# Kernel tuning notes

Hardware: AMD Instinct MI355X
Metric: run time of the kernel (lower is better)

## Reference

```python
import jax, jax.numpy as jnp
import numpy as np

D = 768
H = 12
FF = 3072
B = 64
S = 197
NUM_ITERS = 5
DT = 0.1


def setup_inputs() -> dict:
    key = jax.random.key(0)
    ks = jax.random.split(key, 16)
    sc = 0.02
    inp = {
        'x': jax.random.normal(ks[0], (B, S, D), jnp.float32),
        # MultiheadAttention params (torch layout: in_proj_weight (3D, D))
        'in_proj_w': jax.random.normal(ks[1], (3 * D, D), jnp.float32) * sc,
        'in_proj_b': jnp.zeros((3 * D,), jnp.float32),
        'out_proj_w': jax.random.normal(ks[2], (D, D), jnp.float32) * sc,
        'out_proj_b': jnp.zeros((D,), jnp.float32),
        # LayerNorms
        'ln_attn_g': jnp.ones((D,), jnp.float32),
        'ln_attn_b': jnp.zeros((D,), jnp.float32),
        'ln1_g': jnp.ones((D,), jnp.float32),
        'ln1_b': jnp.zeros((D,), jnp.float32),
        'ln2_g': jnp.ones((D,), jnp.float32),
        'ln2_b': jnp.zeros((D,), jnp.float32),
        # INL dynamics MLP: Linear(D,D) -> GELU -> Linear(D,D)
        'inl_w1': jax.random.normal(ks[3], (D, D), jnp.float32) * sc,
        'inl_b1': jnp.zeros((D,), jnp.float32),
        'inl_w2': jax.random.normal(ks[4], (D, D), jnp.float32) * sc,
        'inl_b2': jnp.zeros((D,), jnp.float32),
        # FFN: Linear(D,FF) -> GELU -> Linear(FF,D)
        'ffn_w1': jax.random.normal(ks[5], (FF, D), jnp.float32) * sc,
        'ffn_b1': jnp.zeros((FF,), jnp.float32),
        'ffn_w2': jax.random.normal(ks[6], (D, FF), jnp.float32) * sc,
        'ffn_b2': jnp.zeros((D,), jnp.float32),
    }
    return inp


def _layernorm(x, g, b, eps=1e-5):
    mu = jnp.mean(x, axis=-1, keepdims=True)
    var = jnp.var(x, axis=-1, keepdims=True)
    return (x - mu) * jax.lax.rsqrt(var + eps) * g + b


def _mha(x, in_w, in_b, out_w, out_b):
    # x: (B,S,D); qkv projection per torch MultiheadAttention
    qkv = jnp.einsum('bsd,ed->bse', x, in_w) + in_b  # (B,S,3D)
    q, k, v = jnp.split(qkv, 3, axis=-1)
    dh = D // H
    q = q.reshape(q.shape[0], q.shape[1], H, dh)
    k = k.reshape(k.shape[0], k.shape[1], H, dh)
    v = v.reshape(v.shape[0], v.shape[1], H, dh)
    scores = jnp.einsum('bqhd,bkhd->bhqk', q, k) / jnp.sqrt(jnp.float32(dh))
    attn = jax.nn.softmax(scores, axis=-1)
    out = jnp.einsum('bhqk,bkhd->bqhd', attn, v)
    out = out.reshape(out.shape[0], out.shape[1], D)
    return jnp.einsum('bsd,ed->bse', out, out_w) + out_b


def _forward(x, in_proj_w, in_proj_b, out_proj_w, out_proj_b,
             ln_attn_g, ln_attn_b, ln1_g, ln1_b, ln2_g, ln2_b,
             inl_w1, inl_b1, inl_w2, inl_b2,
             ffn_w1, ffn_b1, ffn_w2, ffn_b2):
    xn = _layernorm(x, ln_attn_g, ln_attn_b)
    x = x + _mha(xn, in_proj_w, in_proj_b, out_proj_w, out_proj_b)

    # INL dynamics: 5-iter fixed-point loop on normalized state
    state = _layernorm(x, ln1_g, ln1_b)

    def step(state, _):
        h = jax.nn.gelu(jnp.einsum('bsd,ed->bse', state, inl_w1) + inl_b1,
                        approximate=False)
        delta = jnp.einsum('bse,de->bsd', h, inl_w2) + inl_b2
        return state + DT * delta, None

    state, _ = jax.lax.scan(step, state, None, length=NUM_ITERS)
    x = x + state

    # FFN
    xn2 = _layernorm(x, ln2_g, ln2_b)
    h = jax.nn.gelu(jnp.einsum('bsd,fd->bsf', xn2, ffn_w1) + ffn_b1,
                    approximate=False)
    x = x + jnp.einsum('bsf,df->bsd', h, ffn_w2) + ffn_b2
    return x


def reference(x, in_proj_w, in_proj_b, out_proj_w, out_proj_b,
              ln_attn_g, ln_attn_b, ln1_g, ln1_b, ln2_g, ln2_b,
              inl_w1, inl_b1, inl_w2, inl_b2,
              ffn_w1, ffn_b1, ffn_w2, ffn_b2):
    return _forward(x, in_proj_w, in_proj_b, out_proj_w, out_proj_b,
                    ln_attn_g, ln_attn_b, ln1_g, ln1_b, ln2_g, ln2_b,
                    inl_w1, inl_b1, inl_w2, inl_b2,
                    ffn_w1, ffn_b1, ffn_w2, ffn_b2)
```

## Files before the change

### kernel.cpp

```cpp
#include <hip/hip_runtime.h>
#include <hip/hip_bf16.h>
#include <cstdio>

typedef __bf16 bf16x4 __attribute__((ext_vector_type(4)));
typedef __bf16 bf16x8 __attribute__((ext_vector_type(8)));
typedef float  f32x4  __attribute__((ext_vector_type(4)));

#define NTOK 12608
#define DMODEL 768
#define SEQ 197

__device__ __forceinline__ float b2f(__bf16 v) { return (float)v; }

__device__ __forceinline__ float gelu_f(float x) {
    float y = 1.5957691216f * (x + 0.044715f * x * x * x);
    float e = __expf(y);
    float t = 1.f - 2.f / (e + 1.f);
    return 0.5f * x * (1.f + t);
}

__device__ __forceinline__ void gload16(const void* src, void* dst) {
    __builtin_amdgcn_global_load_lds(
        (const __attribute__((address_space(1))) void*)src,
        (__attribute__((address_space(3))) void*)dst,
        16, 0, 0);
}

struct CvtArgs {
    const float* src[6];
    __bf16* dst[6];
    int n4[6];
};
__global__ __launch_bounds__(256) void cvt_all_k(CvtArgs a)
{
#pragma unroll
    for (int t = 0; t < 6; ++t) {
        const float4* in = (const float4*)a.src[t];
        bf16x4* out = (bf16x4*)a.dst[t];
        const int n4 = a.n4[t];
        for (int i = blockIdx.x * 256 + threadIdx.x; i < n4; i += gridDim.x * 256) {
            float4 v = in[i];
            bf16x4 o;
            o[0] = (__bf16)v.x; o[1] = (__bf16)v.y; o[2] = (__bf16)v.z; o[3] = (__bf16)v.w;
            out[i] = o;
        }
    }
}

__global__ __launch_bounds__(256) void ln_k(const float* __restrict__ x,
                                            const float* __restrict__ g,
                                            const float* __restrict__ b,
                                            __bf16* __restrict__ out, int N)
{
    int wid = blockIdx.x * 4 + (threadIdx.x >> 6);
    if (wid >= N) return;
    int lane = threadIdx.x & 63;
    const float4* row = (const float4*)(x + (size_t)wid * DMODEL);
    float v[12];
    float s = 0.f, sq = 0.f;
#pragma unroll
    for (int j = 0; j < 3; ++j) {
        float4 u = row[lane + 64 * j];
        float f0 = u.x, f1 = u.y, f2 = u.z, f3 = u.w;
        v[j*4+0] = f0; v[j*4+1] = f1; v[j*4+2] = f2; v[j*4+3] = f3;
        s += f0 + f1 + f2 + f3;
        sq += f0*f0 + f1*f1 + f2*f2 + f3*f3;
    }
#pragma unroll
    for (int o = 32; o >= 1; o >>= 1) { s += __shfl_xor(s, o); sq += __shfl_xor(sq, o); }
    float mu = s * (1.f / DMODEL);
    float var = sq * (1.f / DMODEL) - mu * mu;
    float rstd = rsqrtf(var + 1e-5f);
    bf16x4* orow = (bf16x4*)(out + (size_t)wid * DMODEL);
    const float4* gg = (const float4*)g;
    const float4* bb = (const float4*)b;
#pragma unroll
    for (int j = 0; j < 3; ++j) {
        float4 gu = gg[lane + 64*j], bu = bb[lane + 64*j];
        bf16x4 o4;
        o4[0] = (__bf16)((v[j*4+0] - mu) * rstd * gu.x + bu.x);
        o4[1] = (__bf16)((v[j*4+1] - mu) * rstd * gu.y + bu.y);
        o4[2] = (__bf16)((v[j*4+2] - mu) * rstd * gu.z + bu.z);
        o4[3] = (__bf16)((v[j*4+3] - mu) * rstd * gu.w + bu.w);
        orow[lane + 64*j] = o4;
    }
}

__global__ __launch_bounds__(256) void addln_k(float* __restrict__ x1,
                                               const __bf16* __restrict__ st,
                                               const float* __restrict__ g,
                                               const float* __restrict__ b,
                                               __bf16* __restrict__ xn2, int N)
{
    int wid = blockIdx.x * 4 + (threadIdx.x >> 6);
    if (wid >= N) return;
    int lane = threadIdx.x & 63;
    float4* r1 = (float4*)(x1 + (size_t)wid * DMODEL);
    const bf16x4* r2 = (const bf16x4*)(st + (size_t)wid * DMODEL);
    float v[12];
    float s = 0.f, sq = 0.f;
#pragma unroll
    for (int j = 0; j < 3; ++j) {
        float4 u1 = r1[lane + 64*j];
        bf16x4 u2 = r2[lane + 64*j];
        float f0 = u1.x + b2f(u2[0]), f1 = u1.y + b2f(u2[1]);
        float f2 = u1.z + b2f(u2[2]), f3 = u1.w + b2f(u2[3]);
        v[j*4+0] = f0; v[j*4+1] = f1; v[j*4+2] = f2; v[j*4+3] = f3;
        s += f0 + f1 + f2 + f3;
        sq += f0*f0 + f1*f1 + f2*f2 + f3*f3;
        float4 o; o.x = f0; o.y = f1; o.z = f2; o.w = f3;
        r1[lane + 64*j] = o;
    }
#pragma unroll
    for (int o = 32; o >= 1; o >>= 1) { s += __shfl_xor(s, o); sq += __shfl_xor(sq, o); }
    float mu = s * (1.f / DMODEL);
    float var = sq * (1.f / DMODEL) - mu * mu;
    float rstd = rsqrtf(var + 1e-5f);
    bf16x4* on = (bf16x4*)(xn2 + (size_t)wid * DMODEL);
    const float4* gg = (const float4*)g;
    const float4* bb = (const float4*)b;
#pragma unroll
    for (int j = 0; j < 3; ++j) {
        float4 gu = gg[lane + 64*j], bu = bb[lane + 64*j];
        bf16x4 o4;
        o4[0] = (__bf16)((v[j*4+0] - mu) * rstd * gu.x + bu.x);
        o4[1] = (__bf16)((v[j*4+1] - mu) * rstd * gu.y + bu.y);
        o4[2] = (__bf16)((v[j*4+2] - mu) * rstd * gu.z + bu.z);
        o4[3] = (__bf16)((v[j*4+3] - mu) * rstd * gu.w + bu.w);
        on[lane + 64*j] = o4;
    }
}

template <int EPI>
__global__ __launch_bounds__(512) void gemm_k(const __bf16* __restrict__ A,
                                              const __bf16* __restrict__ W,
                                              const float* __restrict__ bias,
                                              const void* __restrict__ resv,
                                              void* __restrict__ outv,
                                              int Nv, int K)
{
    __shared__ __align__(16) __bf16 Al[2][64 * 64];
    __shared__ __align__(16) __bf16 Bl[2][128 * 64];
    const int tid = threadIdx.x;
    const int lane = tid & 63;
    const int wv = tid >> 6;
    const int wr = wv >> 2, wc = wv & 3;

    const int ncol = gridDim.x;
    const int nwg = ncol * gridDim.y;
    const int orig = blockIdx.x + ncol * blockIdx.y;
    const int q8 = nwg >> 3, r8 = nwg & 7;
    const int xcd = orig & 7, off8 = orig >> 3;
    const int wgid = (xcd < r8 ? xcd * (q8 + 1) : r8 * (q8 + 1) + (xcd - r8) * q8) + off8;
    const int bcol = (wgid % ncol) * 128;
    const int brow = (wgid / ncol) * 64;

    const int M = ncol * 128;
    const int srow = tid >> 3;
    const int scol = (tid & 7) * 8;
    const int sg = (((tid & 7) ^ (srow & 7)) << 3);
    const int lq = lane >> 4, lr = lane & 15;
    const int gsw = lr & 7;

    int ar = brow + srow; ar = ar < Nv ? ar : (Nv - 1);
    const __bf16* Arow = A + (size_t)ar * K + sg;
    const __bf16* Wrow[2];
#pragma unroll
    for (int it = 0; it < 2; ++it)
        Wrow[it] = W + (size_t)(bcol + it * 64 + srow) * K + sg;

    f32x4 acc[2][2];
#pragma unroll
    for (int m = 0; m < 2; ++m)
#pragma unroll
        for (int n = 0; n < 2; ++n)
#pragma unroll
            for (int i = 0; i < 4; ++i) acc[m][n][i] = 0.f;

    const int nk = K >> 6;

    gload16(Arow, &Al[0][srow * 64 + scol]);
#pragma unroll
    for (int it = 0; it < 2; ++it)
        gload16(Wrow[it], &Bl[0][(it * 64 + srow) * 64 + scol]);
    __syncthreads();

    for (int t = 0; t < nk; ++t) {
        const int cur = t & 1;
        if (t + 1 < nk) {
            const int koff = (t + 1) << 6;
            gload16(Arow + koff, &Al[cur ^ 1][srow * 64 + scol]);
#pragma unroll
            for (int it = 0; it < 2; ++it)
                gload16(Wrow[it] + koff, &Bl[cur ^ 1][(it * 64 + srow) * 64 + scol]);
        }
#pragma unroll
        for (int kk = 0; kk < 2; ++kk) {
            bf16x8 af[2], bfr[2];
            const int cg = ((kk * 4 + lq) ^ gsw) << 3;
#pragma unroll
            for (int m = 0; m < 2; ++m)
                af[m] = *(const bf16x8*)&Al[cur][(wr * 32 + m * 16 + lr) * 64 + cg];
#pragma unroll
            for (int n = 0; n < 2; ++n)
                bfr[n] = *(const bf16x8*)&Bl[cur][(wc * 32 + n * 16 + lr) * 64 + cg];
#pragma unroll
            for (int m = 0; m < 2; ++m)
#pragma unroll
                for (int n = 0; n < 2; ++n)
                    acc[m][n] = __builtin_amdgcn_mfma_f32_16x16x32_bf16(af[m], bfr[n], acc[m][n], 0, 0, 0);
        }
        __syncthreads();
    }

#pragma unroll
    for (int m = 0; m < 2; ++m) {
        int row0 = brow + wr * 32 + m * 16 + lq * 4;
#pragma unroll
        for (int n = 0; n < 2; ++n) {
            int col = bcol + wc * 32 + n * 16 + lr;
            float bv = bias[col];
#pragma unroll
            for (int i = 0; i < 4; ++i) {
                int row = row0 + i;
                if (row < Nv) {
                    float v = acc[m][n][i] + bv;
                    size_t off = (size_t)row * M + col;
                    if constexpr (EPI == 0) {
                        ((__bf16*)outv)[off] = (__bf16)v;
                    } else if constexpr (EPI == 1) {
                        ((float*)outv)[off] = v + ((const float*)resv)[off];
                    } else if constexpr (EPI == 2) {
                        ((__bf16*)outv)[off] = (__bf16)gelu_f(v);
                    } else {
                        ((__bf16*)outv)[off] = (__bf16)(b2f(((const __bf16*)resv)[off]) + 0.1f * v);
                    }
                }
            }
        }
    }
}

template <int EPI>
__global__ __launch_bounds__(512) void gemm_s(const __bf16* __restrict__ A,
                                              const __bf16* __restrict__ W,
                                              const float* __restrict__ bias,
                                              const void* __restrict__ resv,
                                              void* __restrict__ outv,
                                              int Nv, int K)
{
    __shared__ __align__(16) __bf16 Al[2][64 * 64];
    __shared__ __align__(16) __bf16 Bl[2][64 * 64];
    const int tid = threadIdx.x;
    const int lane = tid & 63;
    const int wv = tid >> 6;
    const int wr = wv >> 1, wc = wv & 1;

    const int ncol = gridDim.x;
    const int nwg = ncol * gridDim.y;
    const int orig = blockIdx.x + ncol * blockIdx.y;
    const int q8 = nwg >> 3, r8 = nwg & 7;
    const int xcd = orig & 7, off8 = orig >> 3;
    const int wgid = (xcd < r8 ? xcd * (q8 + 1) : r8 * (q8 + 1) + (xcd - r8) * q8) + off8;
    const int bcol = (wgid % ncol) * 64;
    const int brow = (wgid / ncol) * 64;

    const int M = ncol * 64;
    const int srow = tid >> 3;
    const int scol = (tid & 7) * 8;
    const int sg = (((tid & 7) ^ (srow & 7)) << 3);
    const int lq = lane >> 4, lr = lane & 15;
    const int gsw = lr & 7;

    int ar = brow + srow; ar = ar < Nv ? ar : (Nv - 1);
    const __bf16* Arow = A + (size_t)ar * K + sg;
    const __bf16* Wrow = W + (size_t)(bcol + srow) * K + sg;

    f32x4 acc[2];
#pragma unroll
    for (int n = 0; n < 2; ++n)
#pragma unroll
        for (int i = 0; i < 4; ++i) acc[n][i] = 0.f;

    const int nk = K >> 6;

    gload16(Arow, &Al[0][srow * 64 + scol]);
    gload16(Wrow, &Bl[0][srow * 64 + scol]);
    __syncthreads();

    for (int t = 0; t < nk; ++t) {
        const int cur = t & 1;
        if (t + 1 < nk) {
            const int koff = (t + 1) << 6;
            gload16(Arow + koff, &Al[cur ^ 1][srow * 64 + scol]);
            gload16(Wrow + koff, &Bl[cur ^ 1][srow * 64 + scol]);
        }
#pragma unroll
        for (int kk = 0; kk < 2; ++kk) {
            const int cg = ((kk * 4 + lq) ^ gsw) << 3;
            bf16x8 af = *(const bf16x8*)&Al[cur][(wr * 16 + lr) * 64 + cg];
            bf16x8 bfr[2];
#pragma unroll
            for (int n = 0; n < 2; ++n)
                bfr[n] = *(const bf16x8*)&Bl[cur][(wc * 32 + n * 16 + lr) * 64 + cg];
#pragma unroll
            for (int n = 0; n < 2; ++n)
                acc[n] = __builtin_amdgcn_mfma_f32_16x16x32_bf16(af, bfr[n], acc[n], 0, 0, 0);
        }
        __syncthreads();
    }

    {
        int row0 = brow + wr * 16 + lq * 4;
#pragma unroll
        for (int n = 0; n < 2; ++n) {
            int col = bcol + wc * 32 + n * 16 + lr;
            float bv = bias[col];
#pragma unroll
            for (int i = 0; i < 4; ++i) {
                int row = row0 + i;
                if (row < Nv) {
                    float v = acc[n][i] + bv;
                    size_t off = (size_t)row * M + col;
                    if constexpr (EPI == 0) {
                        ((__bf16*)outv)[off] = (__bf16)v;
                    } else if constexpr (EPI == 1) {
                        ((float*)outv)[off] = v + ((const float*)resv)[off];
                    } else if constexpr (EPI == 2) {
                        ((__bf16*)outv)[off] = (__bf16)gelu_f(v);
                    } else {
                        ((__bf16*)outv)[off] = (__bf16)(b2f(((const __bf16*)resv)[off]) + 0.1f * v);
                    }
                }
            }
        }
    }
}

__global__ __launch_bounds__(256) void attn_k(const __bf16* __restrict__ qkv,
                                              __bf16* __restrict__ attn_out)
{
    constexpr int S = SEQ, LDP = 232, QKVW = 2304;
    __shared__ __align__(16) __bf16 Vt[64 * LDP];
    __shared__ __align__(16) __bf16 P[4][16 * LDP];
    const int bh = blockIdx.x >> 1;
    const int half = blockIdx.x & 1;
    const int b = bh / 12, h = bh % 12;
    const size_t base = (size_t)b * S * QKVW;
    const int tid = threadIdx.x, lane = tid & 63, wv = tid >> 6;
    const int lq = lane >> 4, lr = lane & 15;

    for (int idx = tid; idx < 224 * 8; idx += 256) {
        int j = idx >> 3, d0 = (idx & 7) * 8;
        bf16x8 v8;
        if (j < S) v8 = *(const bf16x8*)(qkv + base + (size_t)j * QKVW + 1536 + h * 64 + d0);
        else {
#pragma unroll
            for (int e = 0; e < 8; ++e) v8[e] = (__bf16)0.f;
        }
#pragma unroll
        for (int e = 0; e < 8; ++e) Vt[(d0 + e) * LDP + j] = v8[e];
    }
    __syncthreads();

    for (int qt = wv + half * 4; qt < 13; qt += 8) {
        int q0 = qt * 16;
        int qrow = q0 + lr; qrow = qrow < S ? qrow : (S - 1);
        bf16x8 aq[2];
#pragma unroll
        for (int kk = 0; kk < 2; ++kk)
            aq[kk] = *(const bf16x8*)(qkv + base + (size_t)qrow * QKVW + h * 64 + kk * 32 + lq * 8);

        f32x4 sc[14];
#pragma unroll
        for (int jf = 0; jf < 14; ++jf) {
#pragma unroll
            for (int i = 0; i < 4; ++i) sc[jf][i] = 0.f;
            int j = jf * 16 + lr; int jc = j < S ? j : (S - 1);
#pragma unroll
            for (int kk = 0; kk < 2; ++kk) {
                bf16x8 bk = *(const bf16x8*)(qkv + base + (size_t)jc * QKVW + 768 + h * 64 + kk * 32 + lq * 8);
                sc[jf] = __builtin_amdgcn_mfma_f32_16x16x32_bf16(aq[kk], bk, sc[jf], 0, 0, 0);
            }
        }
        bool colv[14];
#pragma unroll
        for (int jf = 0; jf < 14; ++jf) colv[jf] = (jf * 16 + lr) < S;
#pragma unroll
        for (int i = 0; i < 4; ++i) {
            float mx = -1.0e30f;
#pragma unroll
            for (int jf = 0; jf < 14; ++jf) {
                float sv = colv[jf] ? sc[jf][i] : -1.0e30f;
                sc[jf][i] = sv;
                mx = fmaxf(mx, sv);
            }
#pragma unroll
            for (int o = 8; o >= 1; o >>= 1) mx = fmaxf(mx, __shfl_xor(mx, o));
            float sm = 0.f;
#pragma unroll
            for (int jf = 0; jf < 14; ++jf) {
                float p = expf((sc[jf][i] - mx) * 0.125f);
                sc[jf][i] = p; sm += p;
            }
#pragma unroll
            for (int o = 8; o >= 1; o >>= 1) sm += __shfl_xor(sm, o);
            float inv = 1.f / sm;
#pragma unroll
            for (int jf = 0; jf < 14; ++jf)
                P[wv][(lq * 4 + i) * LDP + jf * 16 + lr] = (__bf16)(sc[jf][i] * inv);
        }
        f32x4 o4[4];
#pragma unroll
        for (int df = 0; df < 4; ++df)
#pragma unroll
            for (int i = 0; i < 4; ++i) o4[df][i] = 0.f;
#pragma unroll
        for (int ks = 0; ks < 7; ++ks) {
            bf16x8 pa = *(const bf16x8*)&P[wv][lr * LDP + ks * 32 + lq * 8];
#pragma unroll
            for (int df = 0; df < 4; ++df) {
                bf16x8 vb = *(const bf16x8*)&Vt[(df * 16 + lr) * LDP + ks * 32 + lq * 8];
                o4[df] = __builtin_amdgcn_mfma_f32_16x16x32_bf16(pa, vb, o4[df], 0, 0, 0);
            }
        }
#pragma unroll
        for (int df = 0; df < 4; ++df)
#pragma unroll
            for (int i = 0; i < 4; ++i) {
                int qr = q0 + lq * 4 + i;
                if (qr < S)
                    attn_out[((size_t)b * S + qr) * DMODEL + h * 64 + df * 16 + lr] = (__bf16)o4[df][i];
            }
    }
}

extern "C" void kernel_launch(void* const* d_in, const int* in_sizes, int n_in,
                              void* d_out, int out_size, void* d_ws, size_t ws_size,
                              hipStream_t stream) {
    const float* x      = (const float*)d_in[0];
    const float* in_w   = (const float*)d_in[1];
    const float* in_b   = (const float*)d_in[2];
    const float* out_w  = (const float*)d_in[3];
    const float* out_b  = (const float*)d_in[4];
    const float* lnA_g  = (const float*)d_in[5];
    const float* lnA_b  = (const float*)d_in[6];
    const float* ln1_g  = (const float*)d_in[7];
    const float* ln1_b  = (const float*)d_in[8];
    const float* ln2_g  = (const float*)d_in[9];
    const float* ln2_b  = (const float*)d_in[10];
    const float* inl_w1 = (const float*)d_in[11];
    const float* inl_b1 = (const float*)d_in[12];
    const float* inl_w2 = (const float*)d_in[13];
    const float* inl_b2 = (const float*)d_in[14];
    const float* ffn_w1 = (const float*)d_in[15];
    const float* ffn_b1 = (const float*)d_in[16];
    const float* ffn_w2 = (const float*)d_in[17];
    const float* ffn_b2 = (const float*)d_in[18];

    const int N = NTOK;
    const size_t sz_inw = (size_t)2304 * 768, sz_outw = (size_t)768 * 768;
    const size_t sz_i1 = (size_t)768 * 768, sz_i2 = (size_t)768 * 768;
    const size_t sz_f1 = (size_t)3072 * 768, sz_f2 = (size_t)768 * 3072;
    const size_t wtot = sz_inw + sz_outw + sz_i1 + sz_i2 + sz_f1 + sz_f2;

    const size_t bA = (size_t)N * 3072 * 2;
    const size_t bB = (size_t)N * 768 * 2;
    const size_t bS = (size_t)N * 768 * 2;
    const size_t bX = (size_t)N * 768 * 4;
    const size_t need = wtot * 2 + bA + bB + bS + bX;
    if (ws_size < need) {
        fprintf(stderr, "kernel_launch: ws_size %zu < required %zu\n", ws_size, need);
        return;
    }
    char* ws = (char*)d_ws;
    __bf16* w_in  = (__bf16*)ws;
    __bf16* w_out = w_in + sz_inw;
    __bf16* w_i1  = w_out + sz_outw;
    __bf16* w_i2  = w_i1 + sz_i1;
    __bf16* w_f1  = w_i2 + sz_i2;
    __bf16* w_f2  = w_f1 + sz_f1;
    char* p = ws + wtot * 2;
    __bf16* bufA = (__bf16*)p;            p += bA;
    __bf16* bufB = (__bf16*)p;            p += bB;
    __bf16* st   = (__bf16*)p;            p += bS;
    float*  x1   = (float*)p;

    dim3 blk(256), gblk(512);
    const int lnGrid = (N + 3) / 4;
    const int nrow = 197;

    CvtArgs ca;
    ca.src[0] = in_w;   ca.dst[0] = w_in;  ca.n4[0] = (int)(sz_inw / 4);
    ca.src[1] = out_w;  ca.dst[1] = w_out; ca.n4[1] = (int)(sz_outw / 4);
    ca.src[2] = inl_w1; ca.dst[2] = w_i1;  ca.n4[2] = (int)(sz_i1 / 4);
    ca.src[3] = inl_w2; ca.dst[3] = w_i2;  ca.n4[3] = (int)(sz_i2 / 4);
    ca.src[4] = ffn_w1; ca.dst[4] = w_f1;  ca.n4[4] = (int)(sz_f1 / 4);
    ca.src[5] = ffn_w2; ca.dst[5] = w_f2;  ca.n4[5] = (int)(sz_f2 / 4);
    cvt_all_k<<<dim3(1024), blk, 0, stream>>>(ca);

    ln_k<<<dim3(lnGrid), blk, 0, stream>>>(x, lnA_g, lnA_b, bufB, N);
    gemm_k<0><<<dim3(18, nrow), gblk, 0, stream>>>(bufB, w_in, in_b, nullptr, bufA, N, 768);
    attn_k<<<dim3(1536), blk, 0, stream>>>(bufA, bufB);
    gemm_s<1><<<dim3(12, nrow), gblk, 0, stream>>>(bufB, w_out, out_b, x, x1, N, 768);
    ln_k<<<dim3(lnGrid), blk, 0, stream>>>(x1, ln1_g, ln1_b, st, N);
    for (int it = 0; it < 5; ++it) {
        gemm_s<2><<<dim3(12, nrow), gblk, 0, stream>>>(st, w_i1, inl_b1, nullptr, bufA, N, 768);
        gemm_s<3><<<dim3(12, nrow), gblk, 0, stream>>>(bufA, w_i2, inl_b2, st, st, N, 768);
    }
    addln_k<<<dim3(lnGrid), blk, 0, stream>>>(x1, st, ln2_g, ln2_b, bufB, N);
    gemm_k<2><<<dim3(24, nrow), gblk, 0, stream>>>(bufB, w_f1, ffn_b1, nullptr, bufA, N, 768);
    gemm_k<1><<<dim3(6, nrow), gblk, 0, stream>>>(bufA, w_f2, ffn_b2, x1, (float*)d_out, N, 3072);
}
```

Before: 780.2 us.

## Add triple-buffered 128x128 GEMM and re-map GEMM tile sizes per layer

Replaces the small 64x64 GEMM with a 128x128-tile kernel that keeps a three-stage LDS ring, waits on vmcnt explicitly, and raises wave priority around the MFMA block, so global loads overlap compute more deeply. The QKV and FFN GEMMs use this new kernel, and the out-projection and INL loop GEMMs move from the 64x64 kernel to the existing gemm_k with fewer column blocks. Larger tiles improve data reuse and cut launch-grid size, at the cost of more LDS (96KB), lower occupancy, and possible wave-quantization imbalance on the 768-wide GEMMs.

New measurement: 903.1 us. 1.16x slower.

```diff
diff --git a/kernel.cpp b/kernel.cpp
--- a/kernel.cpp
+++ b/kernel.cpp
@@ -242,19 +242,19 @@
 }
 
 template <int EPI>
-__global__ __launch_bounds__(512) void gemm_s(const __bf16* __restrict__ A,
+__global__ __launch_bounds__(512) void gemm_p(const __bf16* __restrict__ A,
                                               const __bf16* __restrict__ W,
                                               const float* __restrict__ bias,
                                               const void* __restrict__ resv,
                                               void* __restrict__ outv,
                                               int Nv, int K)
 {
-    __shared__ __align__(16) __bf16 Al[2][64 * 64];
-    __shared__ __align__(16) __bf16 Bl[2][64 * 64];
+    __shared__ __align__(16) __bf16 Al[3][128 * 64];
+    __shared__ __align__(16) __bf16 Bl[3][128 * 64];
     const int tid = threadIdx.x;
     const int lane = tid & 63;
     const int wv = tid >> 6;
-    const int wr = wv >> 1, wc = wv & 1;
+    const int wr = wv >> 2, wc = wv & 3;
 
     const int ncol = gridDim.x;
     const int nwg = ncol * gridDim.y;
@@ -262,56 +262,89 @@
     const int q8 = nwg >> 3, r8 = nwg & 7;
     const int xcd = orig & 7, off8 = orig >> 3;
     const int wgid = (xcd < r8 ? xcd * (q8 + 1) : r8 * (q8 + 1) + (xcd - r8) * q8) + off8;
-    const int bcol = (wgid % ncol) * 64;
-    const int brow = (wgid / ncol) * 64;
-
-    const int M = ncol * 64;
+    const int bcol = (wgid % ncol) * 128;
+    const int brow = (wgid / ncol) * 128;
+
+    const int M = ncol * 128;
     const int srow = tid >> 3;
     const int scol = (tid & 7) * 8;
     const int sg = (((tid & 7) ^ (srow & 7)) << 3);
     const int lq = lane >> 4, lr = lane & 15;
     const int gsw = lr & 7;
 
-    int ar = brow + srow; ar = ar < Nv ? ar : (Nv - 1);
-    const __bf16* Arow = A + (size_t)ar * K + sg;
-    const __bf16* Wrow = W + (size_t)(bcol + srow) * K + sg;
-
-    f32x4 acc[2];
-#pragma unroll
-    for (int n = 0; n < 2; ++n)
-#pragma unroll
-        for (int i = 0; i < 4; ++i) acc[n][i] = 0.f;
+    const __bf16* Arow[2];
+    const __bf16* Wrow[2];
+#pragma unroll
+    for (int it = 0; it < 2; ++it) {
+        int row = it * 64 + srow;
+        int ar = brow + row; ar = ar < Nv ? ar : (Nv - 1);
+        Arow[it] = A + (size_t)ar * K + sg;
+        Wrow[it] = W + (size_t)(bcol + row) * K + sg;
+    }
+
+    f32x4 acc[4][2];
+#pragma unroll
+    for (int m = 0; m < 4; ++m)
+#pragma unroll
+        for (int n = 0; n < 2; ++n)
+#pragma unroll
+            for (int i = 0; i < 4; ++i) acc[m][n][i] = 0.f;
 
     const int nk = K >> 6;
 
-    gload16(Arow, &Al[0][srow * 64 + scol]);
-    gload16(Wrow, &Bl[0][srow * 64 + scol]);
-    __syncthreads();
+    auto STAGE = [&](int b, int kt) {
+        const int koff = kt << 6;
+#pragma unroll
+        for (int it = 0; it < 2; ++it) {
+            int row = it * 64 + srow;
+            gload16(Arow[it] + koff, &Al[b][row * 64 + scol]);
+            gload16(Wrow[it] + koff, &Bl[b][row * 64 + scol]);
+        }
+    };
+
+    STAGE(0, 0);
+    STAGE(1, 1);
+    int b0 = 0, b1 = 1, b2 = 2;
 
     for (int t = 0; t < nk; ++t) {
-        const int cur = t & 1;
-        if (t + 1 < nk) {
-            const int koff = (t + 1) << 6;
-            gload16(Arow + koff, &Al[cur ^ 1][srow * 64 + scol]);
-            gload16(Wrow + koff, &Bl[cur ^ 1][srow * 64 + scol]);
-        }
+        if (t + 2 < nk) {
+            STAGE(b2, t + 2);
+            asm volatile("s_waitcnt vmcnt(8)" ::: "memory");
+        } else if (t + 1 < nk) {
+            asm volatile("s_waitcnt vmcnt(4)" ::: "memory");
+        } else {
+            asm volatile("s_waitcnt vmcnt(0)" ::: "memory");
+        }
+        __builtin_amdgcn_s_barrier();
+        __builtin_amdgcn_sched_barrier(0);
+
+        __builtin_amdgcn_s_setprio(1);
 #pragma unroll
         for (int kk = 0; kk < 2; ++kk) {
+            bf16x8 af[4], bfr[2];
             const int cg = ((kk * 4 + lq) ^ gsw) << 3;
-            bf16x8 af = *(const bf16x8*)&Al[cur][(wr * 16 + lr) * 64 + cg];
-            bf16x8 bfr[2];
+#pragma unroll
+            for (int m = 0; m < 4; ++m)
+                af[m] = *(const bf16x8*)&Al[b0][(wr * 64 + m * 16 + lr) * 64 + cg];
 #pragma unroll
             for (int n = 0; n < 2; ++n)
-                bfr[n] = *(const bf16x8*)&Bl[cur][(wc * 32 + n * 16 + lr) * 64 + cg];
-#pragma unroll
-            for (int n = 0; n < 2; ++n)
-                acc[n] = __builtin_amdgcn_mfma_f32_16x16x32_bf16(af, bfr[n], acc[n], 0, 0, 0);
-        }
-        __syncthreads();
-    }
-
-    {
-        int row0 = brow + wr * 16 + lq * 4;
+                bfr[n] = *(const bf16x8*)&Bl[b0][(wc * 32 + n * 16 + lr) * 64 + cg];
+#pragma unroll
+            for (int m = 0; m < 4; ++m)
+#pragma unroll
+                for (int n = 0; n < 2; ++n)
+                    acc[m][n] = __builtin_amdgcn_mfma_f32_16x16x32_bf16(af[m], bfr[n], acc[m][n], 0, 0, 0);
+        }
+        __builtin_amdgcn_s_setprio(0);
+
+        __builtin_amdgcn_sched_barrier(0);
+        __builtin_amdgcn_s_barrier();
+        int tmp = b0; b0 = b1; b1 = b2; b2 = tmp;
+    }
+
+#pragma unroll
+    for (int m = 0; m < 4; ++m) {
+        int row0 = brow + wr * 64 + m * 16 + lq * 4;
 #pragma unroll
         for (int n = 0; n < 2; ++n) {
             int col = bcol + wc * 32 + n * 16 + lr;
@@ -320,7 +353,7 @@
             for (int i = 0; i < 4; ++i) {
                 int row = row0 + i;
                 if (row < Nv) {
-                    float v = acc[n][i] + bv;
+                    float v = acc[m][n][i] + bv;
                     size_t off = (size_t)row * M + col;
                     if constexpr (EPI == 0) {
                         ((__bf16*)outv)[off] = (__bf16)v;
@@ -488,7 +521,8 @@
 
     dim3 blk(256), gblk(512);
     const int lnGrid = (N + 3) / 4;
-    const int nrow = 197;
+    const int nrow64 = 197;
+    const int nrow128 = 99;
 
     CvtArgs ca;
     ca.src[0] = in_w;   ca.dst[0] = w_in;  ca.n4[0] = (int)(sz_inw / 4);
@@ -500,15 +534,15 @@
     cvt_all_k<<<dim3(1024), blk, 0, stream>>>(ca);
 
     ln_k<<<dim3(lnGrid), blk, 0, stream>>>(x, lnA_g, lnA_b, bufB, N);
-    gemm_k<0><<<dim3(18, nrow), gblk, 0, stream>>>(bufB, w_in, in_b, nullptr, bufA, N, 768);
+    gemm_p<0><<<dim3(18, nrow128), gblk, 0, stream>>>(bufB, w_in, in_b, nullptr, bufA, N, 768);
     attn_k<<<dim3(1536), blk, 0, stream>>>(bufA, bufB);
-    gemm_s<1><<<dim3(12, nrow), gblk, 0, stream>>>(bufB, w_out, out_b, x, x1, N, 768);
+    gemm_k<1><<<dim3(6, nrow64), gblk, 0, stream>>>(bufB, w_out, out_b, x, x1, N, 768);
     ln_k<<<dim3(lnGrid), blk, 0, stream>>>(x1, ln1_g, ln1_b, st, N);
     for (int it = 0; it < 5; ++it) {
-        gemm_s<2><<<dim3(12, nrow), gblk, 0, stream>>>(st, w_i1, inl_b1, nullptr, bufA, N, 768);
-        gemm_s<3><<<dim3(12, nrow), gblk, 0, stream>>>(bufA, w_i2, inl_b2, st, st, N, 768);
+        gemm_k<2><<<dim3(6, nrow64), gblk, 0, stream>>>(st, w_i1, inl_b1, nullptr, bufA, N, 768);
+        gemm_k<3><<<dim3(6, nrow64), gblk, 0, stream>>>(bufA, w_i2, inl_b2, st, st, N, 768);
     }
     addln_k<<<dim3(lnGrid), blk, 0, stream>>>(x1, st, ln2_g, ln2_b, bufB, N);
-    gemm_k<2><<<dim3(24, nrow), gblk, 0, stream>>>(bufB, w_f1, ffn_b1, nullptr, bufA, N, 768);
-    gemm_k<1><<<dim3(6, nrow), gblk, 0, stream>>>(bufA, w_f2, ffn_b2, x1, (float*)d_out, N, 3072);
-}
+    gemm_p<2><<<dim3(24, nrow128), gblk, 0, stream>>>(bufB, w_f1, ffn_b1, nullptr, bufA, N, 768);
+    gemm_p<1><<<dim3(6, nrow128), gblk, 0, stream>>>(bufA, w_f2, ffn_b2, x1, (float*)d_out, N, 3072);
+}
```
